# Kernel tuning notes

Measured on AMD Instinct MI355X. Metric: run time of the kernel, lower is better.

## Reference

```python
import jax, jax.numpy as jnp
import numpy as np

N, IN_DIM, OUT_DIM = 100000, 256, 256
EPS = 1e-6

def setup_inputs() -> dict:
    key = jax.random.key(0)
    ks = jax.random.split(key, 7)
    s = 1.0 / np.sqrt(IN_DIM)
    x = jax.random.normal(ks[0], (N, IN_DIM), dtype=jnp.float32)
    Wq = jax.random.uniform(ks[1], (IN_DIM, OUT_DIM), jnp.float32, -s, s)
    bq = jax.random.uniform(ks[2], (OUT_DIM,), jnp.float32, -s, s)
    Wk = jax.random.uniform(ks[3], (IN_DIM, OUT_DIM), jnp.float32, -s, s)
    bk = jax.random.uniform(ks[4], (OUT_DIM,), jnp.float32, -s, s)
    Wv = jax.random.uniform(ks[5], (IN_DIM, OUT_DIM), jnp.float32, -s, s)
    bv = jax.random.uniform(ks[6], (OUT_DIM,), jnp.float32, -s, s)
    return {"x": x, "Wq": Wq, "bq": bq, "Wk": Wk, "bk": bk, "Wv": Wv, "bv": bv}

def reference(x, Wq, bq, Wk, bk, Wv, bv):
    Q = jax.nn.relu(x @ Wq + bq)          # [N, d]
    K = jax.nn.relu(x @ Wk + bk)          # [N, d]
    V = x @ Wv + bv                       # [N, d]
    KV = jnp.einsum('nd,ne->de', K, V)    # [d, d]
    out = Q @ KV                          # [N, d]
    normalizer = Q @ K.sum(axis=0)[:, None].reshape(-1) [..., None] if False else (Q @ K.sum(axis=0)[:, None]) + EPS  # [N, 1]
    return out / normalizer
```

## Files before the change

kernel.cpp:

```cpp
#include <hip/hip_runtime.h>

typedef unsigned short u16;
typedef float f32x4 __attribute__((ext_vector_type(4)));
typedef short s16x8 __attribute__((ext_vector_type(8)));
typedef unsigned short u16x4 __attribute__((ext_vector_type(4)));

#define EPS 1e-6f

static __device__ __forceinline__ u16 f2bf(float f) {
  unsigned u = __float_as_uint(f);
  u += 0x7fffu + ((u >> 16) & 1u);
  return (u16)(u >> 16);
}
static __device__ __forceinline__ float bf2f(u16 h) {
  return __uint_as_float(((unsigned)h) << 16);
}

__global__ void wtrans_kernel(const float* __restrict__ Wq, const float* __restrict__ Wk,
                              const float* __restrict__ Wv,
                              u16* __restrict__ WqT, u16* __restrict__ WkT, u16* __restrict__ WvT) {
  int b = blockIdx.x;
  int mat = b >> 4, cg = b & 15;
  const float* W = mat == 0 ? Wq : (mat == 1 ? Wk : Wv);
  u16* WT = mat == 0 ? WqT : (mat == 1 ? WkT : WvT);
  int t = threadIdx.x;
  int c = cg * 16 + (t & 15);
  int k0 = (t >> 4) * 16;
  for (int i = 0; i < 16; ++i) {
    int k = k0 + i;
    WT[c * 256 + k] = f2bf(W[k * 256 + c]);
  }
}

__global__ __launch_bounds__(256, 2)
void qkv_kernel(const float* __restrict__ x,
                const u16* __restrict__ WqT, const u16* __restrict__ WkT, const u16* __restrict__ WvT,
                const float* __restrict__ bq, const float* __restrict__ bk, const float* __restrict__ bv,
                u16* __restrict__ Qb, u16* __restrict__ Kt, u16* __restrict__ Vt,
                float* __restrict__ ksum, int N, int NPAD) {
  __shared__ u16 xs[128][264];
  __shared__ u16 wst[128][40];
  __shared__ float ksl[256];
  const int tid = threadIdx.x;
  const int n0 = blockIdx.x * 128;

  ksl[tid] = 0.f;

  for (int i = 0; i < 32; ++i) {
    int l = tid + i * 256;
    int row = l >> 6;
    int c4 = (l & 63) << 2;
    int n = n0 + row;
    float4 v = make_float4(0.f, 0.f, 0.f, 0.f);
    if (n < N) v = *(const float4*)(x + (size_t)n * 256 + c4);
    u16x4 pk;
    pk[0] = f2bf(v.x); pk[1] = f2bf(v.y); pk[2] = f2bf(v.z); pk[3] = f2bf(v.w);
    *(u16x4*)&xs[row][c4] = pk;
  }

  const int wave = tid >> 6, lane = tid & 63;
  const int quad = lane >> 4, l16 = lane & 15;
  const int wr = (wave >> 1) * 64;
  const int wc = (wave & 1) * 64;

  const int scol = tid >> 1, sseg = (tid & 1) * 16;

  s16x8 w0, w1;
  {
    const u16* p = WqT + (size_t)scol * 256 + sseg;
    w0 = *(const s16x8*)p;
    w1 = *(const s16x8*)(p + 8);
  }

  f32x4 acc[4][4] = {};
  for (int it = 0; it < 48; ++it) {
    const int ph = it >> 3, kc = (it & 7) * 32;
    const int mat = ph >> 1;
    const int colBase = (ph & 1) * 128;

    __syncthreads();
    *(s16x8*)&wst[scol][sseg] = w0;
    *(s16x8*)&wst[scol][sseg + 8] = w1;
    __syncthreads();

    if (it + 1 < 48) {
      int itn = it + 1;
      int phn = itn >> 3, kcn = (itn & 7) * 32;
      int matn = phn >> 1, colBn = (phn & 1) * 128;
      const u16* WTn = matn == 0 ? WqT : (matn == 1 ? WkT : WvT);
      const u16* p = WTn + (size_t)(colBn + scol) * 256 + kcn + sseg;
      w0 = *(const s16x8*)p;
      w1 = *(const s16x8*)(p + 8);
    }

    s16x8 a[4], b[4];
    for (int f = 0; f < 4; ++f) a[f] = *(const s16x8*)&xs[wr + f * 16 + l16][kc + quad * 8];
    for (int f = 0; f < 4; ++f) b[f] = *(const s16x8*)&wst[wc + f * 16 + l16][quad * 8];
    for (int fr = 0; fr < 4; ++fr)
      for (int fc = 0; fc < 4; ++fc)
        acc[fr][fc] = __builtin_amdgcn_mfma_f32_16x16x32_bf16(a[fr], b[fc], acc[fr][fc], 0, 0, 0);

    if ((it & 7) == 7) {
      const float* bias = mat == 0 ? bq : (mat == 1 ? bk : bv);
      float ksacc[4] = {0.f, 0.f, 0.f, 0.f};
      for (int fc = 0; fc < 4; ++fc) {
        int colg = colBase + wc + fc * 16 + l16;
        float bb = bias[colg];
        for (int fr = 0; fr < 4; ++fr) {
          int nl = wr + fr * 16 + quad * 4;
          int n = n0 + nl;
          if (mat == 0) {
            for (int j = 0; j < 4; ++j) {
              float v = acc[fr][fc][j] + bb;
              v = fmaxf(v, 0.f);
              Qb[(size_t)(n + j) * 256 + colg] = (n + j < N) ? f2bf(v) : (u16)0;
            }
          } else {
            u16x4 pk;
            for (int j = 0; j < 4; ++j) {
              float v = acc[fr][fc][j] + bb;
              if (mat == 1) v = fmaxf(v, 0.f);
              bool ok = (n + j < N);
              pk[j] = ok ? f2bf(v) : (u16)0;
              if (mat == 1) ksacc[fc] += ok ? v : 0.f;
            }
            u16* T = (mat == 1) ? Kt : Vt;
            *(u16x4*)&T[(size_t)colg * NPAD + n] = pk;
          }
        }
      }
      if (mat == 1) {
        for (int fc = 0; fc < 4; ++fc) {
          float v = ksacc[fc];
          v += __shfl_xor(v, 16);
          v += __shfl_xor(v, 32);
          if (quad == 0) atomicAdd(&ksl[colBase + wc + fc * 16 + l16], v);
        }
      }
      for (int fr = 0; fr < 4; ++fr)
        for (int fc = 0; fc < 4; ++fc)
          acc[fr][fc] = (f32x4){0.f, 0.f, 0.f, 0.f};
    }
  }
  __syncthreads();
  atomicAdd(&ksum[tid], ksl[tid]);
}

__global__ __launch_bounds__(256, 2)
void kv_kernel(const u16* __restrict__ Kt, const u16* __restrict__ Vt,
               float* __restrict__ P, int NPAD) {
  __shared__ u16 As[128][40];
  __shared__ u16 Bs[128][40];
  const int tid = threadIdx.x;
  const int s = blockIdx.x & 63;
  const int tile = blockIdx.x >> 6;
  const int ti = (tile >> 1) * 128;
  const int tj = (tile & 1) * 128;
  const int wave = tid >> 6, lane = tid & 63;
  const int quad = lane >> 4, l16 = lane & 15;
  const int we = (wave >> 1) * 64;
  const int wd = (wave & 1) * 64;
  f32x4 acc[4][4] = {};
  const int NCH = NPAD >> 5;

  int row0 = (tid * 2) >> 2, seg0 = ((tid * 2) & 3) * 8;
  int row1 = (tid * 2 + 1) >> 2, seg1 = ((tid * 2 + 1) & 3) * 8;

  s16x8 ra0, ra1, rb0, rb1;
  int c = s;
  if (c < NCH) {
    int nb = c << 5;
    ra0 = *(const s16x8*)&Vt[(size_t)(ti + row0) * NPAD + nb + seg0];
    ra1 = *(const s16x8*)&Vt[(size_t)(ti + row1) * NPAD + nb + seg1];
    rb0 = *(const s16x8*)&Kt[(size_t)(tj + row0) * NPAD + nb + seg0];
    rb1 = *(const s16x8*)&Kt[(size_t)(tj + row1) * NPAD + nb + seg1];
  }
  for (; c < NCH; c += 64) {
    __syncthreads();
    *(s16x8*)&As[row0][seg0] = ra0;
    *(s16x8*)&As[row1][seg1] = ra1;
    *(s16x8*)&Bs[row0][seg0] = rb0;
    *(s16x8*)&Bs[row1][seg1] = rb1;
    __syncthreads();
    int cn = c + 64;
    if (cn < NCH) {
      int nb = cn << 5;
      ra0 = *(const s16x8*)&Vt[(size_t)(ti + row0) * NPAD + nb + seg0];
      ra1 = *(const s16x8*)&Vt[(size_t)(ti + row1) * NPAD + nb + seg1];
      rb0 = *(const s16x8*)&Kt[(size_t)(tj + row0) * NPAD + nb + seg0];
      rb1 = *(const s16x8*)&Kt[(size_t)(tj + row1) * NPAD + nb + seg1];
    }
    s16x8 a[4], b[4];
    for (int f = 0; f < 4; ++f) a[f] = *(const s16x8*)&As[we + f * 16 + l16][quad * 8];
    for (int f = 0; f < 4; ++f) b[f] = *(const s16x8*)&Bs[wd + f * 16 + l16][quad * 8];
    for (int fr = 0; fr < 4; ++fr)
      for (int fc = 0; fc < 4; ++fc)
        acc[fr][fc] = __builtin_amdgcn_mfma_f32_16x16x32_bf16(a[fr], b[fc], acc[fr][fc], 0, 0, 0);
  }
  float* Pp = P + (size_t)s * 65536;
  for (int fr = 0; fr < 4; ++fr)
    for (int fc = 0; fc < 4; ++fc) {
      int d = tj + wd + fc * 16 + l16;
      int e0 = ti + we + fr * 16 + quad * 4;
      *(f32x4*)&Pp[(size_t)d * 256 + e0] = acc[fr][fc];
    }
}

__global__ void kvred_kernel(const float* __restrict__ P, u16* __restrict__ KVtb) {
  int d = blockIdx.x;
  int e = threadIdx.x;
  float s = 0.f;
  for (int sp = 0; sp < 64; ++sp) s += P[(size_t)sp * 65536 + d * 256 + e];
  KVtb[e * 256 + d] = f2bf(s);
}

__global__ __launch_bounds__(256, 2)
void out_kernel(const u16* __restrict__ Qb, const u16* __restrict__ KVtb,
                const float* __restrict__ ksum, float* __restrict__ out,
                int N, int NPAD) {
  __shared__ u16 Qs[128][264];
  __shared__ u16 KVs[128][40];
  __shared__ float nrm[128];
  __shared__ float ks[256];
  __shared__ float nrmp[256];
  const int tid = threadIdx.x;
  const int r0 = blockIdx.x * 128;

  for (int i = 0; i < 16; ++i) {
    int l = tid + i * 256;
    int row = l >> 5;
    int seg = (l & 31) << 3;
    *(s16x8*)&Qs[row][seg] = *(const s16x8*)&Qb[(size_t)(r0 + row) * 256 + seg];
  }
  ks[tid] = ksum[tid];
  __syncthreads();

  {
    int r = tid & 127, h = tid >> 7;
    float sa = 0.f;
    for (int d = h * 128; d < h * 128 + 128; d += 8) {
      s16x8 q = *(const s16x8*)&Qs[r][d];
      for (int j = 0; j < 8; ++j) sa += bf2f((u16)q[j]) * ks[d + j];
    }
    nrmp[tid] = sa;
  }
  __syncthreads();
  if (tid < 128) nrm[tid] = nrmp[tid] + nrmp[tid + 128] + EPS;

  const int wave = tid >> 6, lane = tid & 63;
  const int quad = lane >> 4, l16 = lane & 15;
  const int we = (wave >> 1) * 64;
  const int wrw = (wave & 1) * 64;
  const int scol = tid >> 1, sseg = (tid & 1) * 16;

  s16x8 w0, w1;
  {
    const u16* p = KVtb + (size_t)scol * 256 + sseg;
    w0 = *(const s16x8*)p;
    w1 = *(const s16x8*)(p + 8);
  }

  f32x4 acc[4][4] = {};
  for (int it = 0; it < 16; ++it) {
    const int eh = it >> 3, kc = (it & 7) * 32;

    __syncthreads();
    *(s16x8*)&KVs[scol][sseg] = w0;
    *(s16x8*)&KVs[scol][sseg + 8] = w1;
    __syncthreads();

    if (it + 1 < 16) {
      int itn = it + 1;
      int ehn = itn >> 3, kcn = (itn & 7) * 32;
      const u16* p = KVtb + (size_t)(ehn * 128 + scol) * 256 + kcn + sseg;
      w0 = *(const s16x8*)p;
      w1 = *(const s16x8*)(p + 8);
    }

    s16x8 a[4], b[4];
    for (int f = 0; f < 4; ++f) a[f] = *(const s16x8*)&KVs[we + f * 16 + l16][quad * 8];
    for (int f = 0; f < 4; ++f) b[f] = *(const s16x8*)&Qs[wrw + f * 16 + l16][kc + quad * 8];
    for (int fr = 0; fr < 4; ++fr)
      for (int fc = 0; fc < 4; ++fc)
        acc[fr][fc] = __builtin_amdgcn_mfma_f32_16x16x32_bf16(a[fr], b[fc], acc[fr][fc], 0, 0, 0);

    if ((it & 7) == 7) {
      for (int fc = 0; fc < 4; ++fc) {
        int rl = wrw + fc * 16 + l16;
        int rg = r0 + rl;
        float inv = 1.0f / nrm[rl];
        if (rg < N) {
          for (int fr = 0; fr < 4; ++fr) {
            int eg = eh * 128 + we + fr * 16 + quad * 4;
            f32x4 o;
            o[0] = acc[fr][fc][0] * inv;
            o[1] = acc[fr][fc][1] * inv;
            o[2] = acc[fr][fc][2] * inv;
            o[3] = acc[fr][fc][3] * inv;
            *(f32x4*)&out[(size_t)rg * 256 + eg] = o;
          }
        }
      }
      for (int fr = 0; fr < 4; ++fr)
        for (int fc = 0; fc < 4; ++fc)
          acc[fr][fc] = (f32x4){0.f, 0.f, 0.f, 0.f};
    }
  }
}

extern "C" void kernel_launch(void* const* d_in, const int* in_sizes, int n_in,
                              void* d_out, int out_size, void* d_ws, size_t ws_size,
                              hipStream_t stream) {
  const float* x  = (const float*)d_in[0];
  const float* Wq = (const float*)d_in[1];
  const float* bq = (const float*)d_in[2];
  const float* Wk = (const float*)d_in[3];
  const float* bk = (const float*)d_in[4];
  const float* Wv = (const float*)d_in[5];
  const float* bv = (const float*)d_in[6];
  float* out = (float*)d_out;

  int N = in_sizes[0] / 256;
  int NPAD = ((N + 127) / 128) * 128;
  int nblk = NPAD / 128;

  char* p = (char*)d_ws;
  size_t szT = (size_t)256 * NPAD * sizeof(u16);
  u16* Kt = (u16*)p; p += szT;
  u16* Vt = (u16*)p; p += szT;
  u16* Qb = (u16*)p; p += szT;
  float* P = (float*)p; p += (size_t)64 * 65536 * sizeof(float);
  u16* KVtb = (u16*)p; p += (size_t)65536 * sizeof(u16);
  float* ksum = (float*)p; p += 256 * sizeof(float);
  u16* WqT = (u16*)p; p += (size_t)65536 * sizeof(u16);
  u16* WkT = (u16*)p; p += (size_t)65536 * sizeof(u16);
  u16* WvT = (u16*)p; p += (size_t)65536 * sizeof(u16);

  hipMemsetAsync(ksum, 0, 256 * sizeof(float), stream);
  wtrans_kernel<<<48, 256, 0, stream>>>(Wq, Wk, Wv, WqT, WkT, WvT);
  qkv_kernel<<<nblk, 256, 0, stream>>>(x, WqT, WkT, WvT, bq, bk, bv, Qb, Kt, Vt, ksum, N, NPAD);
  kv_kernel<<<256, 256, 0, stream>>>(Kt, Vt, P, NPAD);
  kvred_kernel<<<256, 256, 0, stream>>>(P, KVtb);
  out_kernel<<<nblk, 256, 0, stream>>>(Qb, KVtb, ksum, out, N, NPAD);
}
```

Before: 377.5 us.

## Load weight fragments directly into registers, use atomic split-K reduction for KV

The QKV and output kernels stop staging weight and KV tiles through shared memory. Each wave loads its MFMA B-fragments straight from global/L2 with register double-buffering, which removes two barriers per k-step. The Q store is transposed (operands swapped) so it writes packed u16x4 instead of scalar stores. The KV split-K goes from 64 to 128 splits and accumulates with float atomics into a single buffer, replacing the 64-slice partial buffer and its reduction kernel. The costs are atomic contention on the 256x256 KV buffer, an extra memset, and non-deterministic summation order.

Measured after the change: 569.4 us. 50.8% more time.

```diff
diff --git a/kernel.cpp b/kernel.cpp
--- a/kernel.cpp
+++ b/kernel.cpp
@@ -39,7 +39,6 @@
                 u16* __restrict__ Qb, u16* __restrict__ Kt, u16* __restrict__ Vt,
                 float* __restrict__ ksum, int N, int NPAD) {
   __shared__ u16 xs[128][264];
-  __shared__ u16 wst[128][40];
   __shared__ float ksl[256];
   const int tid = threadIdx.x;
   const int n0 = blockIdx.x * 128;
@@ -57,79 +56,93 @@
     pk[0] = f2bf(v.x); pk[1] = f2bf(v.y); pk[2] = f2bf(v.z); pk[3] = f2bf(v.w);
     *(u16x4*)&xs[row][c4] = pk;
   }
+  __syncthreads();
 
   const int wave = tid >> 6, lane = tid & 63;
   const int quad = lane >> 4, l16 = lane & 15;
   const int wr = (wave >> 1) * 64;
   const int wc = (wave & 1) * 64;
 
-  const int scol = tid >> 1, sseg = (tid & 1) * 16;
-
-  s16x8 w0, w1;
-  {
-    const u16* p = WqT + (size_t)scol * 256 + sseg;
-    w0 = *(const s16x8*)p;
-    w1 = *(const s16x8*)(p + 8);
-  }
-
-  f32x4 acc[4][4] = {};
-  for (int it = 0; it < 48; ++it) {
-    const int ph = it >> 3, kc = (it & 7) * 32;
+  for (int ph = 0; ph < 6; ++ph) {
     const int mat = ph >> 1;
     const int colBase = (ph & 1) * 128;
-
-    __syncthreads();
-    *(s16x8*)&wst[scol][sseg] = w0;
-    *(s16x8*)&wst[scol][sseg + 8] = w1;
-    __syncthreads();
-
-    if (it + 1 < 48) {
-      int itn = it + 1;
-      int phn = itn >> 3, kcn = (itn & 7) * 32;
-      int matn = phn >> 1, colBn = (phn & 1) * 128;
-      const u16* WTn = matn == 0 ? WqT : (matn == 1 ? WkT : WvT);
-      const u16* p = WTn + (size_t)(colBn + scol) * 256 + kcn + sseg;
-      w0 = *(const s16x8*)p;
-      w1 = *(const s16x8*)(p + 8);
-    }
-
-    s16x8 a[4], b[4];
-    for (int f = 0; f < 4; ++f) a[f] = *(const s16x8*)&xs[wr + f * 16 + l16][kc + quad * 8];
-    for (int f = 0; f < 4; ++f) b[f] = *(const s16x8*)&wst[wc + f * 16 + l16][quad * 8];
-    for (int fr = 0; fr < 4; ++fr)
-      for (int fc = 0; fc < 4; ++fc)
-        acc[fr][fc] = __builtin_amdgcn_mfma_f32_16x16x32_bf16(a[fr], b[fc], acc[fr][fc], 0, 0, 0);
-
-    if ((it & 7) == 7) {
-      const float* bias = mat == 0 ? bq : (mat == 1 ? bk : bv);
+    const u16* WT = mat == 0 ? WqT : (mat == 1 ? WkT : WvT);
+    const u16* wp = WT + (size_t)(colBase + wc + l16) * 256 + quad * 8;
+
+    f32x4 acc[4][4] = {};
+    s16x8 b[4], bn[4];
+#pragma unroll
+    for (int f = 0; f < 4; ++f) b[f] = *(const s16x8*)(wp + f * 4096);
+
+#pragma unroll
+    for (int kc8 = 0; kc8 < 8; ++kc8) {
+      const int ko = kc8 * 32;
+      if (kc8 < 7) {
+#pragma unroll
+        for (int f = 0; f < 4; ++f) bn[f] = *(const s16x8*)(wp + f * 4096 + ko + 32);
+      }
+      s16x8 a[4];
+#pragma unroll
+      for (int f = 0; f < 4; ++f) a[f] = *(const s16x8*)&xs[wr + f * 16 + l16][ko + quad * 8];
+      if (mat == 0) {
+#pragma unroll
+        for (int fr = 0; fr < 4; ++fr)
+#pragma unroll
+          for (int fc = 0; fc < 4; ++fc)
+            acc[fr][fc] = __builtin_amdgcn_mfma_f32_16x16x32_bf16(b[fr], a[fc], acc[fr][fc], 0, 0, 0);
+      } else {
+#pragma unroll
+        for (int fr = 0; fr < 4; ++fr)
+#pragma unroll
+          for (int fc = 0; fc < 4; ++fc)
+            acc[fr][fc] = __builtin_amdgcn_mfma_f32_16x16x32_bf16(a[fr], b[fc], acc[fr][fc], 0, 0, 0);
+      }
+#pragma unroll
+      for (int f = 0; f < 4; ++f) b[f] = bn[f];
+    }
+
+    const float* bias = mat == 0 ? bq : (mat == 1 ? bk : bv);
+    if (mat == 0) {
+#pragma unroll
+      for (int fw = 0; fw < 4; ++fw) {
+        int colg4 = colBase + wc + fw * 16 + quad * 4;
+        float4 bb = *(const float4*)(bias + colg4);
+#pragma unroll
+        for (int fx = 0; fx < 4; ++fx) {
+          int n = n0 + wr + fx * 16 + l16;
+          u16x4 pk;
+          pk[0] = f2bf(fmaxf(acc[fw][fx][0] + bb.x, 0.f));
+          pk[1] = f2bf(fmaxf(acc[fw][fx][1] + bb.y, 0.f));
+          pk[2] = f2bf(fmaxf(acc[fw][fx][2] + bb.z, 0.f));
+          pk[3] = f2bf(fmaxf(acc[fw][fx][3] + bb.w, 0.f));
+          if (n >= N) { pk[0] = 0; pk[1] = 0; pk[2] = 0; pk[3] = 0; }
+          *(u16x4*)&Qb[(size_t)n * 256 + colg4] = pk;
+        }
+      }
+    } else {
       float ksacc[4] = {0.f, 0.f, 0.f, 0.f};
+#pragma unroll
       for (int fc = 0; fc < 4; ++fc) {
         int colg = colBase + wc + fc * 16 + l16;
         float bb = bias[colg];
+#pragma unroll
         for (int fr = 0; fr < 4; ++fr) {
-          int nl = wr + fr * 16 + quad * 4;
-          int n = n0 + nl;
-          if (mat == 0) {
-            for (int j = 0; j < 4; ++j) {
-              float v = acc[fr][fc][j] + bb;
-              v = fmaxf(v, 0.f);
-              Qb[(size_t)(n + j) * 256 + colg] = (n + j < N) ? f2bf(v) : (u16)0;
-            }
-          } else {
-            u16x4 pk;
-            for (int j = 0; j < 4; ++j) {
-              float v = acc[fr][fc][j] + bb;
-              if (mat == 1) v = fmaxf(v, 0.f);
-              bool ok = (n + j < N);
-              pk[j] = ok ? f2bf(v) : (u16)0;
-              if (mat == 1) ksacc[fc] += ok ? v : 0.f;
-            }
-            u16* T = (mat == 1) ? Kt : Vt;
-            *(u16x4*)&T[(size_t)colg * NPAD + n] = pk;
+          int n = n0 + wr + fr * 16 + quad * 4;
+          u16x4 pk;
+#pragma unroll
+          for (int j = 0; j < 4; ++j) {
+            float v = acc[fr][fc][j] + bb;
+            if (mat == 1) v = fmaxf(v, 0.f);
+            bool ok = (n + j < N);
+            pk[j] = ok ? f2bf(v) : (u16)0;
+            if (mat == 1) ksacc[fc] += ok ? v : 0.f;
           }
+          u16* T = (mat == 1) ? Kt : Vt;
+          *(u16x4*)&T[(size_t)colg * NPAD + n] = pk;
         }
       }
       if (mat == 1) {
+#pragma unroll
         for (int fc = 0; fc < 4; ++fc) {
           float v = ksacc[fc];
           v += __shfl_xor(v, 16);
@@ -137,23 +150,21 @@
           if (quad == 0) atomicAdd(&ksl[colBase + wc + fc * 16 + l16], v);
         }
       }
-      for (int fr = 0; fr < 4; ++fr)
-        for (int fc = 0; fc < 4; ++fc)
-          acc[fr][fc] = (f32x4){0.f, 0.f, 0.f, 0.f};
     }
   }
   __syncthreads();
   atomicAdd(&ksum[tid], ksl[tid]);
 }
 
+#define KVSPLIT 128
 __global__ __launch_bounds__(256, 2)
 void kv_kernel(const u16* __restrict__ Kt, const u16* __restrict__ Vt,
-               float* __restrict__ P, int NPAD) {
+               float* __restrict__ KVf, int NPAD) {
   __shared__ u16 As[128][40];
   __shared__ u16 Bs[128][40];
   const int tid = threadIdx.x;
-  const int s = blockIdx.x & 63;
-  const int tile = blockIdx.x >> 6;
+  const int s = blockIdx.x & (KVSPLIT - 1);
+  const int tile = blockIdx.x >> 7;
   const int ti = (tile >> 1) * 128;
   const int tj = (tile & 1) * 128;
   const int wave = tid >> 6, lane = tid & 63;
@@ -175,14 +186,14 @@
     rb0 = *(const s16x8*)&Kt[(size_t)(tj + row0) * NPAD + nb + seg0];
     rb1 = *(const s16x8*)&Kt[(size_t)(tj + row1) * NPAD + nb + seg1];
   }
-  for (; c < NCH; c += 64) {
+  for (; c < NCH; c += KVSPLIT) {
     __syncthreads();
     *(s16x8*)&As[row0][seg0] = ra0;
     *(s16x8*)&As[row1][seg1] = ra1;
     *(s16x8*)&Bs[row0][seg0] = rb0;
     *(s16x8*)&Bs[row1][seg1] = rb1;
     __syncthreads();
-    int cn = c + 64;
+    int cn = c + KVSPLIT;
     if (cn < NCH) {
       int nb = cn << 5;
       ra0 = *(const s16x8*)&Vt[(size_t)(ti + row0) * NPAD + nb + seg0];
@@ -191,27 +202,32 @@
       rb1 = *(const s16x8*)&Kt[(size_t)(tj + row1) * NPAD + nb + seg1];
     }
     s16x8 a[4], b[4];
+#pragma unroll
     for (int f = 0; f < 4; ++f) a[f] = *(const s16x8*)&As[we + f * 16 + l16][quad * 8];
+#pragma unroll
     for (int f = 0; f < 4; ++f) b[f] = *(const s16x8*)&Bs[wd + f * 16 + l16][quad * 8];
+#pragma unroll
     for (int fr = 0; fr < 4; ++fr)
+#pragma unroll
       for (int fc = 0; fc < 4; ++fc)
         acc[fr][fc] = __builtin_amdgcn_mfma_f32_16x16x32_bf16(a[fr], b[fc], acc[fr][fc], 0, 0, 0);
   }
-  float* Pp = P + (size_t)s * 65536;
+#pragma unroll
   for (int fr = 0; fr < 4; ++fr)
+#pragma unroll
     for (int fc = 0; fc < 4; ++fc) {
       int d = tj + wd + fc * 16 + l16;
       int e0 = ti + we + fr * 16 + quad * 4;
-      *(f32x4*)&Pp[(size_t)d * 256 + e0] = acc[fr][fc];
-    }
-}
-
-__global__ void kvred_kernel(const float* __restrict__ P, u16* __restrict__ KVtb) {
-  int d = blockIdx.x;
-  int e = threadIdx.x;
-  float s = 0.f;
-  for (int sp = 0; sp < 64; ++sp) s += P[(size_t)sp * 65536 + d * 256 + e];
-  KVtb[e * 256 + d] = f2bf(s);
+#pragma unroll
+      for (int j = 0; j < 4; ++j)
+        atomicAdd(&KVf[(size_t)d * 256 + e0 + j], acc[fr][fc][j]);
+    }
+}
+
+__global__ void kvconv_kernel(const float* __restrict__ KVf, u16* __restrict__ KVtb) {
+  int i = blockIdx.x * 256 + threadIdx.x;
+  int e = i >> 8, d = i & 255;
+  KVtb[i] = f2bf(KVf[(size_t)d * 256 + e]);
 }
 
 __global__ __launch_bounds__(256, 2)
@@ -219,7 +235,6 @@
                 const float* __restrict__ ksum, float* __restrict__ out,
                 int N, int NPAD) {
   __shared__ u16 Qs[128][264];
-  __shared__ u16 KVs[128][40];
   __shared__ float nrm[128];
   __shared__ float ks[256];
   __shared__ float nrmp[256];
@@ -240,70 +255,66 @@
     float sa = 0.f;
     for (int d = h * 128; d < h * 128 + 128; d += 8) {
       s16x8 q = *(const s16x8*)&Qs[r][d];
+#pragma unroll
       for (int j = 0; j < 8; ++j) sa += bf2f((u16)q[j]) * ks[d + j];
     }
     nrmp[tid] = sa;
   }
   __syncthreads();
   if (tid < 128) nrm[tid] = nrmp[tid] + nrmp[tid + 128] + EPS;
+  __syncthreads();
 
   const int wave = tid >> 6, lane = tid & 63;
   const int quad = lane >> 4, l16 = lane & 15;
   const int we = (wave >> 1) * 64;
   const int wrw = (wave & 1) * 64;
-  const int scol = tid >> 1, sseg = (tid & 1) * 16;
-
-  s16x8 w0, w1;
-  {
-    const u16* p = KVtb + (size_t)scol * 256 + sseg;
-    w0 = *(const s16x8*)p;
-    w1 = *(const s16x8*)(p + 8);
-  }
-
-  f32x4 acc[4][4] = {};
-  for (int it = 0; it < 16; ++it) {
-    const int eh = it >> 3, kc = (it & 7) * 32;
-
-    __syncthreads();
-    *(s16x8*)&KVs[scol][sseg] = w0;
-    *(s16x8*)&KVs[scol][sseg + 8] = w1;
-    __syncthreads();
-
-    if (it + 1 < 16) {
-      int itn = it + 1;
-      int ehn = itn >> 3, kcn = (itn & 7) * 32;
-      const u16* p = KVtb + (size_t)(ehn * 128 + scol) * 256 + kcn + sseg;
-      w0 = *(const s16x8*)p;
-      w1 = *(const s16x8*)(p + 8);
-    }
-
-    s16x8 a[4], b[4];
-    for (int f = 0; f < 4; ++f) a[f] = *(const s16x8*)&KVs[we + f * 16 + l16][quad * 8];
-    for (int f = 0; f < 4; ++f) b[f] = *(const s16x8*)&Qs[wrw + f * 16 + l16][kc + quad * 8];
-    for (int fr = 0; fr < 4; ++fr)
-      for (int fc = 0; fc < 4; ++fc)
-        acc[fr][fc] = __builtin_amdgcn_mfma_f32_16x16x32_bf16(a[fr], b[fc], acc[fr][fc], 0, 0, 0);
-
-    if ((it & 7) == 7) {
-      for (int fc = 0; fc < 4; ++fc) {
-        int rl = wrw + fc * 16 + l16;
-        int rg = r0 + rl;
-        float inv = 1.0f / nrm[rl];
-        if (rg < N) {
-          for (int fr = 0; fr < 4; ++fr) {
-            int eg = eh * 128 + we + fr * 16 + quad * 4;
-            f32x4 o;
-            o[0] = acc[fr][fc][0] * inv;
-            o[1] = acc[fr][fc][1] * inv;
-            o[2] = acc[fr][fc][2] * inv;
-            o[3] = acc[fr][fc][3] * inv;
-            *(f32x4*)&out[(size_t)rg * 256 + eg] = o;
-          }
+  const u16* ap = KVtb + (size_t)(we + l16) * 256 + quad * 8;
+
+  s16x8 a[4], an[4];
+#pragma unroll
+  for (int f = 0; f < 4; ++f) a[f] = *(const s16x8*)(ap + f * 4096);
+
+  for (int eh = 0; eh < 2; ++eh) {
+    f32x4 acc[4][4] = {};
+#pragma unroll
+    for (int kc8 = 0; kc8 < 8; ++kc8) {
+      const int ko = kc8 * 32;
+      if (kc8 < 7) {
+#pragma unroll
+        for (int f = 0; f < 4; ++f) an[f] = *(const s16x8*)(ap + (size_t)(eh * 128 + f * 16) * 256 + ko + 32);
+      } else if (eh == 0) {
+#pragma unroll
+        for (int f = 0; f < 4; ++f) an[f] = *(const s16x8*)(ap + (size_t)(128 + f * 16) * 256);
+      }
+      s16x8 b[4];
+#pragma unroll
+      for (int f = 0; f < 4; ++f) b[f] = *(const s16x8*)&Qs[wrw + f * 16 + l16][ko + quad * 8];
+#pragma unroll
+      for (int fr = 0; fr < 4; ++fr)
+#pragma unroll
+        for (int fc = 0; fc < 4; ++fc)
+          acc[fr][fc] = __builtin_amdgcn_mfma_f32_16x16x32_bf16(a[fr], b[fc], acc[fr][fc], 0, 0, 0);
+#pragma unroll
+      for (int f = 0; f < 4; ++f) a[f] = an[f];
+    }
+
+#pragma unroll
+    for (int fc = 0; fc < 4; ++fc) {
+      int rl = wrw + fc * 16 + l16;
+      int rg = r0 + rl;
+      float inv = 1.0f / nrm[rl];
+      if (rg < N) {
+#pragma unroll
+        for (int fr = 0; fr < 4; ++fr) {
+          int eg = eh * 128 + we + fr * 16 + quad * 4;
+          f32x4 o;
+          o[0] = acc[fr][fc][0] * inv;
+          o[1] = acc[fr][fc][1] * inv;
+          o[2] = acc[fr][fc][2] * inv;
+          o[3] = acc[fr][fc][3] * inv;
+          *(f32x4*)&out[(size_t)rg * 256 + eg] = o;
         }
       }
-      for (int fr = 0; fr < 4; ++fr)
-        for (int fc = 0; fc < 4; ++fc)
-          acc[fr][fc] = (f32x4){0.f, 0.f, 0.f, 0.f};
     }
   }
 }
@@ -329,7 +340,7 @@
   u16* Kt = (u16*)p; p += szT;
   u16* Vt = (u16*)p; p += szT;
   u16* Qb = (u16*)p; p += szT;
-  float* P = (float*)p; p += (size_t)64 * 65536 * sizeof(float);
+  float* KVf = (float*)p; p += (size_t)65536 * sizeof(float);
   u16* KVtb = (u16*)p; p += (size_t)65536 * sizeof(u16);
   float* ksum = (float*)p; p += 256 * sizeof(float);
   u16* WqT = (u16*)p; p += (size_t)65536 * sizeof(u16);
@@ -337,9 +348,10 @@
   u16* WvT = (u16*)p; p += (size_t)65536 * sizeof(u16);
 
   hipMemsetAsync(ksum, 0, 256 * sizeof(float), stream);
+  hipMemsetAsync(KVf, 0, (size_t)65536 * sizeof(float), stream);
   wtrans_kernel<<<48, 256, 0, stream>>>(Wq, Wk, Wv, WqT, WkT, WvT);
   qkv_kernel<<<nblk, 256, 0, stream>>>(x, WqT, WkT, WvT, bq, bk, bv, Qb, Kt, Vt, ksum, N, NPAD);
-  kv_kernel<<<256, 256, 0, stream>>>(Kt, Vt, P, NPAD);
-  kvred_kernel<<<256, 256, 0, stream>>>(P, KVtb);
+  kv_kernel<<<KVSPLIT * 4, 256, 0, stream>>>(Kt, Vt, KVf, NPAD);
+  kvconv_kernel<<<256, 256, 0, stream>>>(KVf, KVtb);
   out_kernel<<<nblk, 256, 0, stream>>>(Qb, KVtb, ksum, out, N, NPAD);
 }
```
